# Optimization experiments

Hardware: AMD Instinct MI355X
Metric: run time of the kernel (lower is better)

## Reference

```python
import jax, jax.numpy as jnp
import numpy as np

N_NODES = 50000
N_EDGES = 640000
D_IN = 128
D_HID = 128
D_OUT = 128


def setup_inputs() -> dict:
    key = jax.random.key(0)
    k1, k2, k3, k4 = jax.random.split(key, 4)
    x = jax.random.normal(k1, (N_NODES, D_IN), dtype=jnp.float32)
    edge_index = jax.random.randint(k2, (2, N_EDGES), 0, N_NODES, dtype=jnp.int32)
    W1 = jax.random.normal(k3, (D_IN, D_HID), dtype=jnp.float32) * (1.0 / np.sqrt(D_IN))
    b1 = jnp.zeros((D_HID,), dtype=jnp.float32)
    W2 = jax.random.normal(k4, (D_HID, D_OUT), dtype=jnp.float32) * (1.0 / np.sqrt(D_HID))
    b2 = jnp.zeros((D_OUT,), dtype=jnp.float32)
    return {"x": x, "edge_index": edge_index, "W1": W1, "b1": b1, "W2": W2, "b2": b2}


def gcn_conv(x, edge_index, W, b, num_nodes):
    # PyG GCNConv: add self-loops, symmetric normalization, linear, aggregate, bias.
    loops = jnp.arange(num_nodes, dtype=edge_index.dtype)
    src = jnp.concatenate([edge_index[0], loops])  # source j
    dst = jnp.concatenate([edge_index[1], loops])  # target i
    deg = jax.ops.segment_sum(jnp.ones_like(dst, dtype=x.dtype), dst,
                              num_segments=num_nodes)  # in-degree incl. self-loop
    dinv = jnp.where(deg > 0, jax.lax.rsqrt(deg), 0.0)
    norm = dinv[src] * dinv[dst]  # [E+N]
    h = x @ W  # [N, hidden]
    msg = norm[:, None] * h[src]  # gather + scale
    out = jax.ops.segment_sum(msg, dst, num_segments=num_nodes)  # scatter-add
    return out + b


def reference(x, edge_index, W1, b1, W2, b2):
    h = gcn_conv(x, edge_index, W1, b1, x.shape[0])
    h = jnp.tanh(h)
    return h @ W2 + b2
```

## Files before the change

kernel.cpp:

```cpp
#include <hip/hip_runtime.h>


#define DFEAT 128
#define CAP 48
#define BROWS 32

typedef __attribute__((ext_vector_type(8))) short short8;
typedef __attribute__((ext_vector_type(4))) float float4v;

__device__ __forceinline__ float bflo(unsigned int u) {
    union { unsigned int i; float f; } v; v.i = u << 16; return v.f;
}
__device__ __forceinline__ float bfhi(unsigned int u) {
    union { unsigned int i; float f; } v; v.i = u & 0xffff0000u; return v.f;
}
__device__ __forceinline__ unsigned short f2bf(float f) {
    union { unsigned int i; float f; } v; v.f = f;
    unsigned int r = v.i + 0x7fffu + ((v.i >> 16) & 1u);
    return (unsigned short)(r >> 16);
}
__device__ __forceinline__ unsigned int pack2(float a, float b) {
    return (unsigned int)f2bf(a) | ((unsigned int)f2bf(b) << 16);
}
__device__ __forceinline__ float fast_tanh(float x) {
    float e = __expf(2.0f * x);
    float r = __builtin_amdgcn_rcpf(e + 1.0f);
    return __builtin_fmaf(-2.0f, r, 1.0f);
}

__global__ void k_scatter_conv(const int* __restrict__ src, const int* __restrict__ dst,
                               int* __restrict__ cnt, int* __restrict__ col,
                               const float* __restrict__ x, unsigned int* __restrict__ xb2,
                               const float* __restrict__ W1, const float* __restrict__ W2,
                               unsigned short* __restrict__ w1f, unsigned short* __restrict__ w2f,
                               int e, int n32) {
    int i = blockIdx.x * blockDim.x + threadIdx.x;
    if (i < 2 * DFEAT * DFEAT) {
        int which = i >> 14;
        int idx = i & 16383;
        int k = idx >> 7, nn = idx & 127;
        int f = ((nn >> 4) << 2) + (k >> 5);
        int lane = (nn & 15) | (((k >> 3) & 3) << 4);
        int j = k & 7;
        int o = f * 512 + lane * 8 + j;
        if (which == 0) w1f[o] = f2bf(W1[idx]);
        else            w2f[o] = f2bf(W2[idx]);
    }
    if (i < e) {
        int d = dst[i];
        int p = atomicAdd(&cnt[d], 1);
        if (p < CAP) col[d * CAP + p] = src[i];
    }
    if (i < n32) {
        float4 v = ((const float4*)x)[i];
        xb2[i * 2]     = pack2(v.x, v.y);
        xb2[i * 2 + 1] = pack2(v.z, v.w);
    }
}

__global__ __launch_bounds__(256) void k_agg_gemm(
    const uint4* __restrict__ xb4, const int* __restrict__ cnt,
    const int* __restrict__ col,
    const unsigned short* __restrict__ w1f, const float* __restrict__ b1,
    const unsigned short* __restrict__ w2f, const float* __restrict__ b2,
    float* __restrict__ out, int n) {
    __shared__ unsigned short aggs[BROWS * 136];
    __shared__ unsigned short hs[BROWS * 136];
    const int t = threadIdx.x;

    const int lane16 = t & 15;
    const int sub = t >> 4;
    for (int g = 0; g < BROWS / 16; ++g) {
        int node_local = g * 16 + sub;
        int node = blockIdx.x * BROWS + node_local;
        int nodec = min(node, n - 1);
        int raw = cnt[nodec];
        int deg = min(raw, CAP);
        float di = rsqrtf((float)(raw + 1));
        uint4 v = xb4[(size_t)nodec * 16 + lane16];
        float a0 = bflo(v.x) * di, a1 = bfhi(v.x) * di;
        float a2 = bflo(v.y) * di, a3 = bfhi(v.y) * di;
        float a4 = bflo(v.z) * di, a5 = bfhi(v.z) * di;
        float a6 = bflo(v.w) * di, a7 = bfhi(v.w) * di;
        const int4* col4 = (const int4*)(col + (size_t)nodec * CAP);
        int nq = (deg + 3) >> 2;
        int4 s4 = col4[0];
        for (int q = 0; q < nq; ++q) {
            int4 nx = col4[min(q + 1, nq - 1)];
            int b4i = q * 4;
            bool c1 = (b4i + 1) < deg, c2 = (b4i + 2) < deg, c3 = (b4i + 3) < deg;
            int i0 = s4.x;
            int i1 = c1 ? s4.y : i0;
            int i2 = c2 ? s4.z : i0;
            int i3 = c3 ? s4.w : i0;
            float d0 = rsqrtf((float)(cnt[i0] + 1));
            float d1 = c1 ? rsqrtf((float)(cnt[i1] + 1)) : 0.f;
            float d2 = c2 ? rsqrtf((float)(cnt[i2] + 1)) : 0.f;
            float d3 = c3 ? rsqrtf((float)(cnt[i3] + 1)) : 0.f;
            uint4 u0 = xb4[(size_t)i0 * 16 + lane16];
            uint4 u1 = xb4[(size_t)i1 * 16 + lane16];
            uint4 u2 = xb4[(size_t)i2 * 16 + lane16];
            uint4 u3 = xb4[(size_t)i3 * 16 + lane16];
            a0 = __builtin_fmaf(bflo(u0.x), d0, a0); a1 = __builtin_fmaf(bfhi(u0.x), d0, a1);
            a2 = __builtin_fmaf(bflo(u0.y), d0, a2); a3 = __builtin_fmaf(bfhi(u0.y), d0, a3);
            a4 = __builtin_fmaf(bflo(u0.z), d0, a4); a5 = __builtin_fmaf(bfhi(u0.z), d0, a5);
            a6 = __builtin_fmaf(bflo(u0.w), d0, a6); a7 = __builtin_fmaf(bfhi(u0.w), d0, a7);
            a0 = __builtin_fmaf(bflo(u1.x), d1, a0); a1 = __builtin_fmaf(bfhi(u1.x), d1, a1);
            a2 = __builtin_fmaf(bflo(u1.y), d1, a2); a3 = __builtin_fmaf(bfhi(u1.y), d1, a3);
            a4 = __builtin_fmaf(bflo(u1.z), d1, a4); a5 = __builtin_fmaf(bfhi(u1.z), d1, a5);
            a6 = __builtin_fmaf(bflo(u1.w), d1, a6); a7 = __builtin_fmaf(bfhi(u1.w), d1, a7);
            a0 = __builtin_fmaf(bflo(u2.x), d2, a0); a1 = __builtin_fmaf(bfhi(u2.x), d2, a1);
            a2 = __builtin_fmaf(bflo(u2.y), d2, a2); a3 = __builtin_fmaf(bfhi(u2.y), d2, a3);
            a4 = __builtin_fmaf(bflo(u2.z), d2, a4); a5 = __builtin_fmaf(bfhi(u2.z), d2, a5);
            a6 = __builtin_fmaf(bflo(u2.w), d2, a6); a7 = __builtin_fmaf(bfhi(u2.w), d2, a7);
            a0 = __builtin_fmaf(bflo(u3.x), d3, a0); a1 = __builtin_fmaf(bfhi(u3.x), d3, a1);
            a2 = __builtin_fmaf(bflo(u3.y), d3, a2); a3 = __builtin_fmaf(bfhi(u3.y), d3, a3);
            a4 = __builtin_fmaf(bflo(u3.z), d3, a4); a5 = __builtin_fmaf(bfhi(u3.z), d3, a5);
            a6 = __builtin_fmaf(bflo(u3.w), d3, a6); a7 = __builtin_fmaf(bfhi(u3.w), d3, a7);
            s4 = nx;
        }
        uint4 o;
        o.x = pack2(a0 * di, a1 * di);
        o.y = pack2(a2 * di, a3 * di);
        o.z = pack2(a4 * di, a5 * di);
        o.w = pack2(a6 * di, a7 * di);
        *(uint4*)&aggs[node_local * 136 + lane16 * 8] = o;
    }
    __syncthreads();

    const int wave = t >> 6, l = t & 63;
    const int strip = wave >> 1;
    const int colh = wave & 1;
    const int kq = l >> 4;
    const int lc = l & 15;
    const int row_local = strip * 16 + lc;

    float4v acc[4];
    for (int ct = 0; ct < 4; ++ct) acc[ct] = (float4v){0.f, 0.f, 0.f, 0.f};
    for (int kc = 0; kc < 4; ++kc) {
        short8 a = *(const short8*)(aggs + row_local * 136 + kc * 32 + kq * 8);
        for (int ct = 0; ct < 4; ++ct) {
            int ctg = colh * 4 + ct;
            short8 b = *(const short8*)(w1f + (ctg * 4 + kc) * 512 + l * 8);
            acc[ct] = __builtin_amdgcn_mfma_f32_16x16x32_bf16(a, b, acc[ct], 0, 0, 0);
        }
    }
    const int drow0 = strip * 16 + kq * 4;
    for (int ct = 0; ct < 4; ++ct) {
        int c = colh * 64 + ct * 16 + lc;
        float bb = b1[c];
        for (int r = 0; r < 4; ++r) {
            float v = fast_tanh(acc[ct][r] + bb);
            hs[(drow0 + r) * 136 + c] = f2bf(v);
        }
    }
    __syncthreads();

    float4v acc2[4];
    for (int ct = 0; ct < 4; ++ct) acc2[ct] = (float4v){0.f, 0.f, 0.f, 0.f};
    for (int kc = 0; kc < 4; ++kc) {
        short8 a = *(const short8*)(hs + row_local * 136 + kc * 32 + kq * 8);
        for (int ct = 0; ct < 4; ++ct) {
            int ctg = colh * 4 + ct;
            short8 b = *(const short8*)(w2f + (ctg * 4 + kc) * 512 + l * 8);
            acc2[ct] = __builtin_amdgcn_mfma_f32_16x16x32_bf16(a, b, acc2[ct], 0, 0, 0);
        }
    }
    const int orow0 = blockIdx.x * BROWS + drow0;
    for (int ct = 0; ct < 4; ++ct) {
        int c = colh * 64 + ct * 16 + lc;
        float bb = b2[c];
        for (int r = 0; r < 4; ++r) {
            int orow = orow0 + r;
            if (orow < n) out[(size_t)orow * DFEAT + c] = acc2[ct][r] + bb;
        }
    }
}

static inline size_t align256(size_t v) { return (v + 255) & ~(size_t)255; }

extern "C" void kernel_launch(void* const* d_in, const int* in_sizes, int n_in,
                              void* d_out, int out_size, void* d_ws, size_t ws_size,
                              hipStream_t stream) {
    const float* x  = (const float*)d_in[0];
    const int*   ei = (const int*)d_in[1];
    const float* W1 = (const float*)d_in[2];
    const float* b1 = (const float*)d_in[3];
    const float* W2 = (const float*)d_in[4];
    const float* b2 = (const float*)d_in[5];
    float* out = (float*)d_out;

    const int N = in_sizes[0] / DFEAT;
    const int E = in_sizes[1] / 2;
    const int* src = ei;
    const int* dst = ei + E;

    char* ws = (char*)d_ws;
    size_t off = 0;
    int* cnt = (int*)(ws + off);  off += align256((size_t)N * 4);
    int* col = (int*)(ws + off);  off += align256((size_t)N * CAP * 4);
    unsigned short* xb  = (unsigned short*)(ws + off); off += align256((size_t)N * DFEAT * 2);
    unsigned short* w1f = (unsigned short*)(ws + off); off += align256((size_t)DFEAT * DFEAT * 2);
    unsigned short* w2f = (unsigned short*)(ws + off); off += align256((size_t)DFEAT * DFEAT * 2);

    const int n32 = N * 32;
    int total = n32 > E ? n32 : E;
    if (total < 2 * DFEAT * DFEAT) total = 2 * DFEAT * DFEAT;

    hipMemsetAsync(cnt, 0, (size_t)N * 4, stream);
    k_scatter_conv<<<(total + 255) / 256, 256, 0, stream>>>(
        src, dst, cnt, col, x, (unsigned int*)xb, W1, W2, w1f, w2f, E, n32);
    k_agg_gemm<<<(N + BROWS - 1) / BROWS, 256, 0, stream>>>(
        (const uint4*)xb, cnt, col, w1f, b1, w2f, b2, out, N);
}
```

Before: 165.1 us.

## Partition edge buckets by block to cut atomic contention; precompute dinv table

Edges are bucketed into 8 partitions chosen by block index, each with its own per-node counter and 16-slot list, which spreads atomics across more addresses. A new descriptor kernel packs the eight partition counts per node and precomputes dinv, adding a zero dummy node so padded lanes gather zeros without branches. The aggregation loads the first quad of all partitions up front, then loops over the remainder. This adds a kernel launch, a larger memset and col array, and more always-issued gathers for low-degree nodes. The per-neighbor degree lookups now read a precomputed float instead of recomputing rsqrt from the count.

After: 173.9 us. 5.3% more time.

```diff
diff --git a/kernel.cpp b/kernel.cpp
--- a/kernel.cpp
+++ b/kernel.cpp
@@ -2,7 +2,8 @@
 
 
 #define DFEAT 128
-#define CAP 48
+#define CAP8 16
+#define NPART 8
 #define BROWS 32
 
 typedef __attribute__((ext_vector_type(8))) short short8;
@@ -28,12 +29,12 @@
     return __builtin_fmaf(-2.0f, r, 1.0f);
 }
 
-__global__ void k_scatter_conv(const int* __restrict__ src, const int* __restrict__ dst,
-                               int* __restrict__ cnt, int* __restrict__ col,
-                               const float* __restrict__ x, unsigned int* __restrict__ xb2,
-                               const float* __restrict__ W1, const float* __restrict__ W2,
-                               unsigned short* __restrict__ w1f, unsigned short* __restrict__ w2f,
-                               int e, int n32) {
+__global__ void k1_scatter_conv(const int* __restrict__ src, const int* __restrict__ dst,
+                                int* __restrict__ cnt8, int* __restrict__ col8,
+                                const float* __restrict__ x, unsigned int* __restrict__ xb2,
+                                const float* __restrict__ W1, const float* __restrict__ W2,
+                                unsigned short* __restrict__ w1f, unsigned short* __restrict__ w2f,
+                                int e, int n32, int n) {
     int i = blockIdx.x * blockDim.x + threadIdx.x;
     if (i < 2 * DFEAT * DFEAT) {
         int which = i >> 14;
@@ -47,26 +48,55 @@
         else            w2f[o] = f2bf(W2[idx]);
     }
     if (i < e) {
+        int p = blockIdx.x & (NPART - 1);
         int d = dst[i];
-        int p = atomicAdd(&cnt[d], 1);
-        if (p < CAP) col[d * CAP + p] = src[i];
+        int cell = p * n + d;
+        int q = atomicAdd(&cnt8[cell], 1);
+        if (q < CAP8) col8[(size_t)cell * CAP8 + q] = src[i];
     }
     if (i < n32) {
         float4 v = ((const float4*)x)[i];
         xb2[i * 2]     = pack2(v.x, v.y);
         xb2[i * 2 + 1] = pack2(v.z, v.w);
+    } else if (i < n32 + 32) {
+        xb2[i * 2] = 0u;
+        xb2[i * 2 + 1] = 0u;
+    }
+}
+
+__global__ void k2_desc(const int* __restrict__ cnt8, uint2* __restrict__ pcnt,
+                        float* __restrict__ dinv, int n) {
+    int i = blockIdx.x * blockDim.x + threadIdx.x;
+    if (i < n) {
+        unsigned int lo = 0, hi = 0;
+        int tot = 0;
+        #pragma unroll
+        for (int p = 0; p < 4; ++p) {
+            int c = min(cnt8[p * n + i], CAP8);
+            tot += c; lo |= (unsigned int)c << (8 * p);
+        }
+        #pragma unroll
+        for (int p = 4; p < 8; ++p) {
+            int c = min(cnt8[p * n + i], CAP8);
+            tot += c; hi |= (unsigned int)c << (8 * (p - 4));
+        }
+        pcnt[i] = make_uint2(lo, hi);
+        dinv[i] = rsqrtf((float)(tot + 1));
+    } else if (i == n) {
+        dinv[n] = 0.f;
     }
 }
 
 __global__ __launch_bounds__(256) void k_agg_gemm(
-    const uint4* __restrict__ xb4, const int* __restrict__ cnt,
-    const int* __restrict__ col,
+    const uint4* __restrict__ xb4, const uint2* __restrict__ pcnt,
+    const float* __restrict__ dinv_t, const int* __restrict__ col8,
     const unsigned short* __restrict__ w1f, const float* __restrict__ b1,
     const unsigned short* __restrict__ w2f, const float* __restrict__ b2,
     float* __restrict__ out, int n) {
     __shared__ unsigned short aggs[BROWS * 136];
     __shared__ unsigned short hs[BROWS * 136];
     const int t = threadIdx.x;
+    const int4* c8 = (const int4*)col8;
 
     const int lane16 = t & 15;
     const int sub = t >> 4;
@@ -74,29 +104,27 @@
         int node_local = g * 16 + sub;
         int node = blockIdx.x * BROWS + node_local;
         int nodec = min(node, n - 1);
-        int raw = cnt[nodec];
-        int deg = min(raw, CAP);
-        float di = rsqrtf((float)(raw + 1));
+        uint2 pc = pcnt[nodec];
+        float di = dinv_t[nodec];
         uint4 v = xb4[(size_t)nodec * 16 + lane16];
         float a0 = bflo(v.x) * di, a1 = bfhi(v.x) * di;
         float a2 = bflo(v.y) * di, a3 = bfhi(v.y) * di;
         float a4 = bflo(v.z) * di, a5 = bfhi(v.z) * di;
         float a6 = bflo(v.w) * di, a7 = bfhi(v.w) * di;
-        const int4* col4 = (const int4*)(col + (size_t)nodec * CAP);
-        int nq = (deg + 3) >> 2;
-        int4 s4 = col4[0];
-        for (int q = 0; q < nq; ++q) {
-            int4 nx = col4[min(q + 1, nq - 1)];
-            int b4i = q * 4;
-            bool c1 = (b4i + 1) < deg, c2 = (b4i + 2) < deg, c3 = (b4i + 3) < deg;
-            int i0 = s4.x;
-            int i1 = c1 ? s4.y : i0;
-            int i2 = c2 ? s4.z : i0;
-            int i3 = c3 ? s4.w : i0;
-            float d0 = rsqrtf((float)(cnt[i0] + 1));
-            float d1 = c1 ? rsqrtf((float)(cnt[i1] + 1)) : 0.f;
-            float d2 = c2 ? rsqrtf((float)(cnt[i2] + 1)) : 0.f;
-            float d3 = c3 ? rsqrtf((float)(cnt[i3] + 1)) : 0.f;
+
+        int4 s[NPART];
+        #pragma unroll
+        for (int p = 0; p < NPART; ++p)
+            s[p] = c8[(size_t)(p * n + nodec) * 4];
+
+        #pragma unroll
+        for (int p = 0; p < NPART; ++p) {
+            int dp = (int)((p < 4 ? (pc.x >> (8 * p)) : (pc.y >> (8 * (p - 4)))) & 0xffu);
+            int i0 = dp > 0 ? s[p].x : n;
+            int i1 = dp > 1 ? s[p].y : n;
+            int i2 = dp > 2 ? s[p].z : n;
+            int i3 = dp > 3 ? s[p].w : n;
+            float d0 = dinv_t[i0], d1 = dinv_t[i1], d2 = dinv_t[i2], d3 = dinv_t[i3];
             uint4 u0 = xb4[(size_t)i0 * 16 + lane16];
             uint4 u1 = xb4[(size_t)i1 * 16 + lane16];
             uint4 u2 = xb4[(size_t)i2 * 16 + lane16];
@@ -117,7 +145,38 @@
             a2 = __builtin_fmaf(bflo(u3.y), d3, a2); a3 = __builtin_fmaf(bfhi(u3.y), d3, a3);
             a4 = __builtin_fmaf(bflo(u3.z), d3, a4); a5 = __builtin_fmaf(bfhi(u3.z), d3, a5);
             a6 = __builtin_fmaf(bflo(u3.w), d3, a6); a7 = __builtin_fmaf(bfhi(u3.w), d3, a7);
-            s4 = nx;
+        }
+        #pragma unroll
+        for (int p = 0; p < NPART; ++p) {
+            int dp = (int)((p < 4 ? (pc.x >> (8 * p)) : (pc.y >> (8 * (p - 4)))) & 0xffu);
+            for (int b = 4; b < dp; b += 4) {
+                int4 sq = c8[(size_t)(p * n + nodec) * 4 + (b >> 2)];
+                int i0 = sq.x;
+                int i1 = (b + 1) < dp ? sq.y : n;
+                int i2 = (b + 2) < dp ? sq.z : n;
+                int i3 = (b + 3) < dp ? sq.w : n;
+                float d0 = dinv_t[i0], d1 = dinv_t[i1], d2 = dinv_t[i2], d3 = dinv_t[i3];
+                uint4 u0 = xb4[(size_t)i0 * 16 + lane16];
+                uint4 u1 = xb4[(size_t)i1 * 16 + lane16];
+                uint4 u2 = xb4[(size_t)i2 * 16 + lane16];
+                uint4 u3 = xb4[(size_t)i3 * 16 + lane16];
+                a0 = __builtin_fmaf(bflo(u0.x), d0, a0); a1 = __builtin_fmaf(bfhi(u0.x), d0, a1);
+                a2 = __builtin_fmaf(bflo(u0.y), d0, a2); a3 = __builtin_fmaf(bfhi(u0.y), d0, a3);
+                a4 = __builtin_fmaf(bflo(u0.z), d0, a4); a5 = __builtin_fmaf(bfhi(u0.z), d0, a5);
+                a6 = __builtin_fmaf(bflo(u0.w), d0, a6); a7 = __builtin_fmaf(bfhi(u0.w), d0, a7);
+                a0 = __builtin_fmaf(bflo(u1.x), d1, a0); a1 = __builtin_fmaf(bfhi(u1.x), d1, a1);
+                a2 = __builtin_fmaf(bflo(u1.y), d1, a2); a3 = __builtin_fmaf(bfhi(u1.y), d1, a3);
+                a4 = __builtin_fmaf(bflo(u1.z), d1, a4); a5 = __builtin_fmaf(bfhi(u1.z), d1, a5);
+                a6 = __builtin_fmaf(bflo(u1.w), d1, a6); a7 = __builtin_fmaf(bfhi(u1.w), d1, a7);
+                a0 = __builtin_fmaf(bflo(u2.x), d2, a0); a1 = __builtin_fmaf(bfhi(u2.x), d2, a1);
+                a2 = __builtin_fmaf(bflo(u2.y), d2, a2); a3 = __builtin_fmaf(bfhi(u2.y), d2, a3);
+                a4 = __builtin_fmaf(bflo(u2.z), d2, a4); a5 = __builtin_fmaf(bfhi(u2.z), d2, a5);
+                a6 = __builtin_fmaf(bflo(u2.w), d2, a6); a7 = __builtin_fmaf(bfhi(u2.w), d2, a7);
+                a0 = __builtin_fmaf(bflo(u3.x), d3, a0); a1 = __builtin_fmaf(bfhi(u3.x), d3, a1);
+                a2 = __builtin_fmaf(bflo(u3.y), d3, a2); a3 = __builtin_fmaf(bfhi(u3.y), d3, a3);
+                a4 = __builtin_fmaf(bflo(u3.z), d3, a4); a5 = __builtin_fmaf(bfhi(u3.z), d3, a5);
+                a6 = __builtin_fmaf(bflo(u3.w), d3, a6); a7 = __builtin_fmaf(bfhi(u3.w), d3, a7);
+            }
         }
         uint4 o;
         o.x = pack2(a0 * di, a1 * di);
@@ -197,19 +256,23 @@
 
     char* ws = (char*)d_ws;
     size_t off = 0;
-    int* cnt = (int*)(ws + off);  off += align256((size_t)N * 4);
-    int* col = (int*)(ws + off);  off += align256((size_t)N * CAP * 4);
-    unsigned short* xb  = (unsigned short*)(ws + off); off += align256((size_t)N * DFEAT * 2);
+    int* cnt8 = (int*)(ws + off);   off += align256((size_t)NPART * N * 4);
+    int* col8 = (int*)(ws + off);   off += align256((size_t)NPART * N * CAP8 * 4);
+    uint2* pcnt = (uint2*)(ws + off); off += align256((size_t)N * 8);
+    float* dinv = (float*)(ws + off); off += align256((size_t)(N + 1) * 4);
+    unsigned short* xb  = (unsigned short*)(ws + off); off += align256((size_t)(N + 1) * DFEAT * 2);
     unsigned short* w1f = (unsigned short*)(ws + off); off += align256((size_t)DFEAT * DFEAT * 2);
     unsigned short* w2f = (unsigned short*)(ws + off); off += align256((size_t)DFEAT * DFEAT * 2);
 
     const int n32 = N * 32;
-    int total = n32 > E ? n32 : E;
-    if (total < 2 * DFEAT * DFEAT) total = 2 * DFEAT * DFEAT;
-
-    hipMemsetAsync(cnt, 0, (size_t)N * 4, stream);
-    k_scatter_conv<<<(total + 255) / 256, 256, 0, stream>>>(
-        src, dst, cnt, col, x, (unsigned int*)xb, W1, W2, w1f, w2f, E, n32);
+    int t1 = n32 + 32;
+    if (t1 < E) t1 = E;
+    if (t1 < 2 * DFEAT * DFEAT) t1 = 2 * DFEAT * DFEAT;
+
+    hipMemsetAsync(cnt8, 0, (size_t)NPART * N * 4, stream);
+    k1_scatter_conv<<<(t1 + 255) / 256, 256, 0, stream>>>(
+        src, dst, cnt8, col8, x, (unsigned int*)xb, W1, W2, w1f, w2f, E, n32, N);
+    k2_desc<<<(N + 1 + 255) / 256, 256, 0, stream>>>(cnt8, pcnt, dinv, N);
     k_agg_gemm<<<(N + BROWS - 1) / BROWS, 256, 0, stream>>>(
-        (const uint4*)xb, cnt, col, w1f, b1, w2f, b2, out, N);
-}
+        (const uint4*)xb, pcnt, dinv, col8, w1f, b1, w2f, b2, out, N);
+}
```
